# Kernel optimization log

Hardware: AMD Instinct MI355X
Metric: run time of the kernel (lower is better)

Reference implementation:

```python
import jax, jax.numpy as jnp
import numpy as np

B, S, H = 64, 256, 768          # batch, seq, feature_size
A = 8                            # atten_num (heads)
GNUM, GSZ = 8192, 64             # group_num, labels per group
LABELS = GNUM * GSZ              # 524288
E = 256                          # args.hidden_size (label embed dim)
TOPK = 10                        # candidates_topk


def setup_inputs() -> dict:
    key = jax.random.key(0)
    ks = jax.random.split(key, 6)
    sc = lambda d: 1.0 / np.sqrt(d)
    return {
        "inputs": jax.random.normal(ks[0], (B, S, H), jnp.float32),
        "W_att": jax.random.normal(ks[1], (A, H), jnp.float32) * sc(H),
        "b_att": jnp.zeros((A,), jnp.float32),
        "W_clf": jax.random.normal(ks[2], (GNUM, H), jnp.float32) * sc(H),
        "b_clf": jnp.zeros((GNUM,), jnp.float32),
        "W_enc": jax.random.normal(ks[3], (E, H), jnp.float32) * sc(H),
        "b_enc": jnp.zeros((E,), jnp.float32),
        "embed_table": jax.random.normal(ks[4], (LABELS, E), jnp.float32) * sc(E),
        "group_y": jnp.arange(LABELS, dtype=jnp.int32).reshape(GNUM, GSZ),
    }


def reference(inputs, W_att, b_att, W_clf, b_clf, W_enc, b_enc, embed_table, group_y):
    # MulitAttention: [B,S,H] -> atten [B,A,S] -> softmax over S -> out [B,A,H]
    atten = jnp.einsum("bsh,ah->bas", inputs, W_att) + b_att[None, :, None]
    atten_sm = jax.nn.softmax(atten, axis=-1)
    out = jnp.einsum("bas,bsh->bah", atten_sm, inputs)

    # group classifier + MaxPool1d over heads -> c_out [B, GNUM]
    group_logits = jnp.einsum("bah,gh->bag", out, W_clf) + b_clf
    c_out = jnp.max(group_logits, axis=1)

    # get_candidates (inference path): sigmoid on detached logits, topk groups,
    # gather group members (fixed group size -> regular [B, TOPK*GSZ])
    probs = jax.nn.sigmoid(jax.lax.stop_gradient(c_out))
    scores, indices = jax.lax.top_k(probs, TOPK)            # [B, TOPK]
    candidates = group_y[indices].reshape(B, TOPK * GSZ)    # [B, C]
    group_candidates_scores = jnp.repeat(scores, GSZ, axis=1)  # [B, C]

    # label scoring: encoder(out) [B,A,E], embed gather [B,C,E],
    # batched dot products [B,A,C], maxpool over heads -> l_out [B,C]
    emb = jnp.einsum("bah,eh->bae", out, W_enc) + b_enc
    embed_weights = embed_table[candidates]                 # [B, C, E]
    logits = jnp.einsum("bce,bae->bac", embed_weights, emb)
    l_out = jnp.max(logits, axis=1)

    return c_out, l_out, candidates, group_candidates_scores
```

## Files before the change

kernel.cpp:

```cpp
#include <hip/hip_runtime.h>

#define B_    64
#define S_    256
#define H_    768
#define A_    8
#define GNUM_ 8192
#define GSZ_  64
#define E_    256
#define TOPK_ 10
#define C_    (TOPK_*GSZ_)
#define BROWS (GNUM_ + E_)

typedef short  bf16x8 __attribute__((ext_vector_type(8)));
typedef float  f32x4  __attribute__((ext_vector_type(4)));

__device__ __forceinline__ ushort f2bf(float x) {
    union { float f; unsigned u; } c; c.f = x;
    unsigned r = c.u + 0x7fff + ((c.u >> 16) & 1);
    return (ushort)(r >> 16);
}
__device__ __forceinline__ float bf2f(ushort h) {
    union { float f; unsigned u; } c; c.u = ((unsigned)h) << 16;
    return c.f;
}
__device__ __forceinline__ float asf(unsigned u) {
    union { unsigned u; float f; } c; c.u = u; return c.f;
}
__device__ __forceinline__ unsigned cvt_pk_bf16(float a, float b) {
    unsigned r;
    asm("v_cvt_pk_bf16_f32 %0, %1, %2" : "=v"(r) : "v"(a), "v"(b));
    return r;
}

__global__ __launch_bounds__(256) void attn1_kernel(
    const float* __restrict__ x, const float* __restrict__ Watt,
    const float* __restrict__ batt, float* __restrict__ attT)
{
    const int b  = blockIdx.x;
    const int s0 = blockIdx.y * 64;
    const int t  = threadIdx.x;
    const int sl = t & 63;
    const int g  = __builtin_amdgcn_readfirstlane(t >> 6);
    __shared__ float Xt[64][65];
    __shared__ float Pp[8][64][5];

    const float* xb = x + ((size_t)b * S_ + s0) * H_;
    float acc[A_] = {};

    for (int h0 = 0; h0 < H_; h0 += 64) {
        __syncthreads();
#pragma unroll
        for (int i = 0; i < 4; i++) {
            int fid = i * 256 + t;
            int r = fid >> 4;
            int c = (fid & 15) * 4;
            float4 v = *(const float4*)(xb + (size_t)r * H_ + h0 + c);
            Xt[r][c] = v.x; Xt[r][c+1] = v.y; Xt[r][c+2] = v.z; Xt[r][c+3] = v.w;
        }
        __syncthreads();
        const float* wp = Watt + h0 + g * 16;
#pragma unroll
        for (int h = 0; h < 16; h++) {
            float xv = Xt[sl][g * 16 + h];
#pragma unroll
            for (int a = 0; a < A_; a++) acc[a] += xv * wp[a * H_ + h];
        }
    }
#pragma unroll
    for (int a = 0; a < A_; a++) Pp[a][sl][g] = acc[a];
    __syncthreads();
#pragma unroll
    for (int i = 0; i < 2; i++) {
        int idx = i * 256 + t;
        int a = idx >> 6, s = idx & 63;
        float v = Pp[a][s][0] + Pp[a][s][1] + Pp[a][s][2] + Pp[a][s][3] + batt[a];
        attT[(size_t)b * (S_*A_) + (size_t)(s0 + s) * A_ + a] = v;
    }
}

__global__ __launch_bounds__(256) void attn2s_kernel(
    const float* __restrict__ x, const float* __restrict__ attT,
    ushort* __restrict__ Ah, ushort* __restrict__ Al)
{
    const int b = blockIdx.x, h0 = blockIdx.y * 256, t = threadIdx.x;
    __shared__ float La[S_ * A_];
    __shared__ float Wsm[A_][260];

#pragma unroll
    for (int i = 0; i < 2; i++) {
        int fid = i * 256 + t;
        *(float4*)&La[fid * 4] =
            *(const float4*)(attT + (size_t)b * (S_*A_) + (size_t)fid * 4);
    }
    __syncthreads();

    {
        const int a = t >> 5, l = t & 31;
        float mx = -1e30f;
#pragma unroll
        for (int k = 0; k < 8; k++) mx = fmaxf(mx, La[(l + 32*k) * A_ + a]);
#pragma unroll
        for (int off = 16; off >= 1; off >>= 1) mx = fmaxf(mx, __shfl_xor(mx, off));
        float ev[8]; float sm = 0.f;
#pragma unroll
        for (int k = 0; k < 8; k++) { ev[k] = expf(La[(l + 32*k) * A_ + a] - mx); sm += ev[k]; }
#pragma unroll
        for (int off = 16; off >= 1; off >>= 1) sm += __shfl_xor(sm, off);
        float inv = 1.f / sm;
#pragma unroll
        for (int k = 0; k < 8; k++) Wsm[a][l + 32*k] = ev[k] * inv;
    }
    __syncthreads();

    const float* xb = x + (size_t)b * S_ * H_ + h0 + t;
    float o[A_] = {};
    for (int s0 = 0; s0 < S_; s0 += 4) {
        float xv0 = xb[(size_t)(s0 + 0) * H_];
        float xv1 = xb[(size_t)(s0 + 1) * H_];
        float xv2 = xb[(size_t)(s0 + 2) * H_];
        float xv3 = xb[(size_t)(s0 + 3) * H_];
#pragma unroll
        for (int a = 0; a < A_; a++) {
            float4 w = *(const float4*)&Wsm[a][s0];
            o[a] += w.x * xv0 + w.y * xv1 + w.z * xv2 + w.w * xv3;
        }
    }
#pragma unroll
    for (int a = 0; a < A_; a++) {
        float v = o[a];
        ushort hi = f2bf(v);
        ushort lo = f2bf(v - bf2f(hi));
        size_t off = (size_t)(b * 8 + a) * H_ + h0 + t;
        Ah[off] = hi; Al[off] = lo;
    }
}

__global__ __launch_bounds__(256, 1) void gemm_mfma_kernel(
    const ushort* __restrict__ Ah, const ushort* __restrict__ Al,
    const float* __restrict__ Wclf, const float* __restrict__ Wenc,
    const float* __restrict__ bclf, const float* __restrict__ benc,
    float* __restrict__ c_out, float* __restrict__ emb)
{
    const int f = blockIdx.x;
    const int xcd = f & 7, s = f >> 3;
    const int p = xcd + 8 * (s >> 2);
    const int m = s & 3;
    if (p >= BROWS / 128) return;
    const int n0 = p * 128, m0 = m * 128;

    __shared__ __align__(16) ushort lds[2][4][128 * 32];
    const int t = threadIdx.x;
    const int w = t >> 6, l = t & 63;
    const int mq = (w & 1) * 64, nq = (w >> 1) * 64;

    const int srow = t >> 2, skc = t & 3;
    const int wr_idx = ((srow * 32 + skc * 8) ^ ((srow & 7) << 3));
    const ushort* baseAh = Ah + (size_t)m0 * H_;
    const ushort* baseAl = Al + (size_t)m0 * H_;
    const float*  baseB  = (n0 < GNUM_) ? (Wclf + (size_t)n0 * H_)
                                        : (Wenc + (size_t)(n0 - GNUM_) * H_);

    uint4  stA[2][2];
    float4 stB[2][2];
    auto loadk = [&](int k0) {
        size_t oA = (size_t)srow * H_ + k0 + skc * 8;
        stA[0][0] = *(const uint4*)(baseAh + oA);
        stA[0][1] = *(const uint4*)(baseAh + oA + (size_t)64 * H_);
        stA[1][0] = *(const uint4*)(baseAl + oA);
        stA[1][1] = *(const uint4*)(baseAl + oA + (size_t)64 * H_);
        const float* bp0 = baseB + (size_t)srow * H_ + k0 + skc * 8;
        const float* bp1 = bp0 + (size_t)64 * H_;
        stB[0][0] = *(const float4*)(bp0);
        stB[0][1] = *(const float4*)(bp0 + 4);
        stB[1][0] = *(const float4*)(bp1);
        stB[1][1] = *(const float4*)(bp1 + 4);
    };

    f32x4 acc[4][4] = {};
    loadk(0);
    const int kc = l >> 4, lr = l & 15;

    for (int kt = 0; kt < H_ / 32; ++kt) {
        ushort* bufp = &lds[kt & 1][0][0];
#pragma unroll
        for (int xx = 0; xx < 2; xx++) {
            *(uint4*)(bufp + xx * 4096 + wr_idx)        = stA[xx][0];
            *(uint4*)(bufp + xx * 4096 + 2048 + wr_idx) = stA[xx][1];
        }
#pragma unroll
        for (int rp = 0; rp < 2; rp++) {
            float fv[8] = { stB[rp][0].x, stB[rp][0].y, stB[rp][0].z, stB[rp][0].w,
                            stB[rp][1].x, stB[rp][1].y, stB[rp][1].z, stB[rp][1].w };
            uint4 hi, lo;
            unsigned* hip = (unsigned*)&hi;
            unsigned* lop = (unsigned*)&lo;
#pragma unroll
            for (int j = 0; j < 4; j++) {
                unsigned pk = cvt_pk_bf16(fv[2*j], fv[2*j+1]);
                hip[j] = pk;
                float r0 = fv[2*j]   - asf(pk << 16);
                float r1 = fv[2*j+1] - asf(pk & 0xffff0000u);
                lop[j] = cvt_pk_bf16(r0, r1);
            }
            *(uint4*)(bufp + 2 * 4096 + rp * 2048 + wr_idx) = hi;
            *(uint4*)(bufp + 3 * 4096 + rp * 2048 + wr_idx) = lo;
        }
        __syncthreads();
        if (kt + 1 < H_ / 32) loadk((kt + 1) * 32);

        bf16x8 fah[4], fal[4], fbh[4], fbl[4];
#pragma unroll
        for (int mt = 0; mt < 4; mt++) {
            int r = mq + mt * 16 + lr;
            int idx = ((r * 32 + kc * 8) ^ ((r & 7) << 3));
            fah[mt] = *(const bf16x8*)(bufp + idx);
            fal[mt] = *(const bf16x8*)(bufp + 4096 + idx);
        }
#pragma unroll
        for (int nt = 0; nt < 4; nt++) {
            int r = nq + nt * 16 + lr;
            int idx = ((r * 32 + kc * 8) ^ ((r & 7) << 3));
            fbh[nt] = *(const bf16x8*)(bufp + 2 * 4096 + idx);
            fbl[nt] = *(const bf16x8*)(bufp + 3 * 4096 + idx);
        }
#pragma unroll
        for (int mt = 0; mt < 4; mt++)
#pragma unroll
            for (int nt = 0; nt < 4; nt++) {
                acc[mt][nt] = __builtin_amdgcn_mfma_f32_16x16x32_bf16(fah[mt], fbh[nt], acc[mt][nt], 0, 0, 0);
                acc[mt][nt] = __builtin_amdgcn_mfma_f32_16x16x32_bf16(fal[mt], fbh[nt], acc[mt][nt], 0, 0, 0);
                acc[mt][nt] = __builtin_amdgcn_mfma_f32_16x16x32_bf16(fah[mt], fbl[nt], acc[mt][nt], 0, 0, 0);
            }
    }

    const int q = l >> 4;
    if (n0 < GNUM_) {
#pragma unroll
        for (int mt = 0; mt < 4; mt++)
#pragma unroll
            for (int nt = 0; nt < 4; nt++) {
                f32x4 a = acc[mt][nt];
                float v = fmaxf(fmaxf(a[0], a[1]), fmaxf(a[2], a[3]));
                v = fmaxf(v, __shfl_xor(v, 16));
                if ((q & 1) == 0) {
                    int mg = m0 + mq + mt * 16 + (q >> 1) * 8;
                    int n  = n0 + nq + nt * 16 + lr;
                    c_out[(size_t)(mg >> 3) * GNUM_ + n] = v + bclf[n];
                }
            }
    } else {
#pragma unroll
        for (int mt = 0; mt < 4; mt++)
#pragma unroll
            for (int nt = 0; nt < 4; nt++) {
                int n = n0 - GNUM_ + nq + nt * 16 + lr;
                float bn = benc[n];
#pragma unroll
                for (int r2 = 0; r2 < 4; r2++) {
                    int mg = m0 + mq + mt * 16 + q * 4 + r2;
                    emb[(size_t)mg * E_ + n] = acc[mt][nt][r2] + bn;
                }
            }
    }
}

__global__ __launch_bounds__(256) void topk_kernel(
    const float* __restrict__ c_out, const int* __restrict__ gy,
    float* __restrict__ cand_f, float* __restrict__ gcs, int* __restrict__ cand_i)
{
    const int b = blockIdx.x, t = threadIdx.x;
    const int lane = t & 63, wv = t >> 6;
    __shared__ float bvv[4]; __shared__ int bii[4];
    __shared__ float topv[TOPK_]; __shared__ int topi[TOPK_];

    const float* row = c_out + (size_t)b * GNUM_;
    float lv[TOPK_]; int li[TOPK_];
#pragma unroll
    for (int k = 0; k < TOPK_; k++) { lv[k] = -1.f; li[k] = 0x7fffffff; }

    for (int i = t; i < GNUM_; i += 256) {
        float p = 1.f / (1.f + expf(-row[i]));
        if (p > lv[TOPK_ - 1]) {
            float cv = p; int ci = i;
#pragma unroll
            for (int k = 0; k < TOPK_; k++) {
                bool sw = (cv > lv[k]);
                float tv = sw ? lv[k] : cv; int ti = sw ? li[k] : ci;
                lv[k] = sw ? cv : lv[k];    li[k] = sw ? ci : li[k];
                cv = tv; ci = ti;
            }
        }
    }

    for (int rnd = 0; rnd < TOPK_; rnd++) {
        float bv = lv[0]; int bi = li[0];
#pragma unroll
        for (int off = 32; off >= 1; off >>= 1) {
            float ov = __shfl_xor(bv, off); int oi = __shfl_xor(bi, off);
            if (ov > bv || (ov == bv && oi < bi)) { bv = ov; bi = oi; }
        }
        if (lane == 0) { bvv[wv] = bv; bii[wv] = bi; }
        __syncthreads();
        float gbv = bvv[0]; int gbi = bii[0];
#pragma unroll
        for (int w = 1; w < 4; w++) {
            float ov = bvv[w]; int oi = bii[w];
            if (ov > gbv || (ov == gbv && oi < gbi)) { gbv = ov; gbi = oi; }
        }
        if (t == 0) { topv[rnd] = gbv; topi[rnd] = gbi; }
        if (li[0] == gbi) {
#pragma unroll
            for (int k = 0; k < TOPK_ - 1; k++) { lv[k] = lv[k + 1]; li[k] = li[k + 1]; }
            lv[TOPK_ - 1] = -1.f; li[TOPK_ - 1] = 0x7fffffff;
        }
        __syncthreads();
    }

    for (int j = t; j < C_; j += 256) {
        int k = j >> 6, slot = j & 63;
        int gi = topi[k];
        int lbl = gy[gi * GSZ_ + slot];
        cand_f[(size_t)b * C_ + j] = (float)lbl;
        gcs[(size_t)b * C_ + j] = topv[k];
        cand_i[b * C_ + j] = lbl;
    }
}

__global__ __launch_bounds__(256) void score_kernel(
    const float* __restrict__ embw, const float* __restrict__ et,
    const int* __restrict__ cand, float* __restrict__ l_out)
{
    const int b = blockIdx.x, c00 = blockIdx.y * 64, t = threadIdx.x;
    __shared__ float el[A_ * E_];
#pragma unroll
    for (int i = 0; i < 2; i++) {
        int fid = i * 256 + t;
        *(float4*)&el[fid * 4] = *(const float4*)(embw + (size_t)b * (A_*E_) + fid * 4);
    }
    __syncthreads();
    const int lane = t & 63, wv = t >> 6, q = lane >> 4, sub = lane & 15;

    int c = c00 + wv * 4 + q;
    const float* er = et + (size_t)cand[b * C_ + c] * E_ + sub * 4;
    float4 v0 = *(const float4*)(er);
    float4 v1 = *(const float4*)(er + 64);
    float4 v2 = *(const float4*)(er + 128);
    float4 v3 = *(const float4*)(er + 192);

    for (int it = 0; it < 4; it++) {
        float4 n0, n1, n2, n3;
        if (it + 1 < 4) {
            int cn = c00 + (it + 1) * 16 + wv * 4 + q;
            const float* ern = et + (size_t)cand[b * C_ + cn] * E_ + sub * 4;
            n0 = *(const float4*)(ern);
            n1 = *(const float4*)(ern + 64);
            n2 = *(const float4*)(ern + 128);
            n3 = *(const float4*)(ern + 192);
        }
        float best = -1e30f;
#pragma unroll
        for (int a = 0; a < A_; a++) {
            const float* ep = el + a * E_ + sub * 4;
            float4 w0 = *(const float4*)(ep);
            float4 w1 = *(const float4*)(ep + 64);
            float4 w2 = *(const float4*)(ep + 128);
            float4 w3 = *(const float4*)(ep + 192);
            float p = v0.x*w0.x + v0.y*w0.y + v0.z*w0.z + v0.w*w0.w
                    + v1.x*w1.x + v1.y*w1.y + v1.z*w1.z + v1.w*w1.w
                    + v2.x*w2.x + v2.y*w2.y + v2.z*w2.z + v2.w*w2.w
                    + v3.x*w3.x + v3.y*w3.y + v3.z*w3.z + v3.w*w3.w;
#pragma unroll
            for (int off = 8; off >= 1; off >>= 1) p += __shfl_xor(p, off);
            best = fmaxf(best, p);
        }
        if (sub == 0) l_out[(size_t)b * C_ + c00 + it * 16 + wv * 4 + q] = best;
        v0 = n0; v1 = n1; v2 = n2; v3 = n3;
    }
}

extern "C" void kernel_launch(void* const* d_in, const int* in_sizes, int n_in,
                              void* d_out, int out_size, void* d_ws, size_t ws_size,
                              hipStream_t stream)
{
    (void)in_sizes; (void)n_in; (void)out_size; (void)ws_size;
    const float* x    = (const float*)d_in[0];
    const float* Watt = (const float*)d_in[1];
    const float* batt = (const float*)d_in[2];
    const float* Wclf = (const float*)d_in[3];
    const float* bclf = (const float*)d_in[4];
    const float* Wenc = (const float*)d_in[5];
    const float* benc = (const float*)d_in[6];
    const float* et   = (const float*)d_in[7];
    const int*   gy   = (const int*)d_in[8];

    float* out    = (float*)d_out;
    float* c_out  = out;
    float* l_out  = out + (size_t)B_ * GNUM_;
    float* cand_f = l_out + (size_t)B_ * C_;
    float* gcs    = cand_f + (size_t)B_ * C_;

    char* ws = (char*)d_ws;
    float*  attT  = (float*) (ws);
    float*  embw  = (float*) (ws + 524288);
    int*    candi = (int*)   (ws + 1048576);
    ushort* Ahw   = (ushort*)(ws + 1212416);
    ushort* Alw   = (ushort*)(ws + 1998848);

    attn1_kernel<<<dim3(B_, 4), 256, 0, stream>>>(x, Watt, batt, attT);
    attn2s_kernel<<<dim3(B_, 3), 256, 0, stream>>>(x, attT, Ahw, Alw);
    gemm_mfma_kernel<<<288, 256, 0, stream>>>(Ahw, Alw, Wclf, Wenc, bclf, benc, c_out, embw);
    topk_kernel<<<B_, 256, 0, stream>>>(c_out, gy, cand_f, gcs, candi);
    score_kernel<<<dim3(B_, 10), 256, 0, stream>>>(embw, et, candi, l_out);
}
```

Measured before the change: 153.9 us.

## Fuse per-tile top-k into GEMM epilogue, merge topk with scoring, add prefetching

The GEMM epilogue now computes sigmoid and a per-128-column top-10 for each batch row and writes the partial candidates. A new scoretop kernel merges the 64 partial lists per batch, gathers the candidates and scores them, replacing the separate topk and score kernels. The GEMM grid shrinks to 256 blocks, and the 8 encoder tiles are claimed through an atomic work queue whose counter is reset in attn1. attn1 and attn2s gain register prefetching of x. This removes a full pass over c_out and one launch, but adds serial warp-level top-k work to the GEMM tail and repeats the top-k merge in each of the 4 blocks per batch.

```diff
diff --git a/kernel.cpp b/kernel.cpp
--- a/kernel.cpp
+++ b/kernel.cpp
@@ -9,7 +9,6 @@
 #define E_    256
 #define TOPK_ 10
 #define C_    (TOPK_*GSZ_)
-#define BROWS (GNUM_ + E_)
 
 typedef short  bf16x8 __attribute__((ext_vector_type(8)));
 typedef float  f32x4  __attribute__((ext_vector_type(4)));
@@ -34,11 +33,14 @@
 
 __global__ __launch_bounds__(256) void attn1_kernel(
     const float* __restrict__ x, const float* __restrict__ Watt,
-    const float* __restrict__ batt, float* __restrict__ attT)
+    const float* __restrict__ batt, float* __restrict__ attT,
+    unsigned* __restrict__ qcnt)
 {
     const int b  = blockIdx.x;
     const int s0 = blockIdx.y * 64;
     const int t  = threadIdx.x;
+    if (b == 0 && blockIdx.y == 0 && t == 0)
+        __hip_atomic_store(qcnt, 0u, __ATOMIC_RELAXED, __HIP_MEMORY_SCOPE_AGENT);
     const int sl = t & 63;
     const int g  = __builtin_amdgcn_readfirstlane(t >> 6);
     __shared__ float Xt[64][65];
@@ -46,18 +48,30 @@
 
     const float* xb = x + ((size_t)b * S_ + s0) * H_;
     float acc[A_] = {};
-
+    int pr[4], pc[4];
+    float4 pref[4];
+#pragma unroll
+    for (int i = 0; i < 4; i++) {
+        int fid = i * 256 + t;
+        pr[i] = fid >> 4; pc[i] = (fid & 15) * 4;
+    }
+#pragma unroll
+    for (int i = 0; i < 4; i++)
+        pref[i] = *(const float4*)(xb + (size_t)pr[i] * H_ + pc[i]);
     for (int h0 = 0; h0 < H_; h0 += 64) {
         __syncthreads();
 #pragma unroll
         for (int i = 0; i < 4; i++) {
-            int fid = i * 256 + t;
-            int r = fid >> 4;
-            int c = (fid & 15) * 4;
-            float4 v = *(const float4*)(xb + (size_t)r * H_ + h0 + c);
-            Xt[r][c] = v.x; Xt[r][c+1] = v.y; Xt[r][c+2] = v.z; Xt[r][c+3] = v.w;
+            float4 v = pref[i];
+            float* dst = &Xt[pr[i]][pc[i]];
+            dst[0] = v.x; dst[1] = v.y; dst[2] = v.z; dst[3] = v.w;
         }
         __syncthreads();
+        if (h0 + 64 < H_) {
+#pragma unroll
+            for (int i = 0; i < 4; i++)
+                pref[i] = *(const float4*)(xb + (size_t)pr[i] * H_ + h0 + 64 + pc[i]);
+        }
         const float* wp = Watt + h0 + g * 16;
 #pragma unroll
         for (int h = 0; h < 16; h++) {
@@ -72,9 +86,9 @@
 #pragma unroll
     for (int i = 0; i < 2; i++) {
         int idx = i * 256 + t;
-        int a = idx >> 6, s = idx & 63;
-        float v = Pp[a][s][0] + Pp[a][s][1] + Pp[a][s][2] + Pp[a][s][3] + batt[a];
-        attT[(size_t)b * (S_*A_) + (size_t)(s0 + s) * A_ + a] = v;
+        int a = idx >> 6, s2 = idx & 63;
+        float v = Pp[a][s2][0] + Pp[a][s2][1] + Pp[a][s2][2] + Pp[a][s2][3] + batt[a];
+        attT[(size_t)b * (S_*A_) + (size_t)(s0 + s2) * A_ + a] = v;
     }
 }
 
@@ -84,7 +98,7 @@
 {
     const int b = blockIdx.x, h0 = blockIdx.y * 256, t = threadIdx.x;
     __shared__ float La[S_ * A_];
-    __shared__ float Wsm[A_][260];
+    __shared__ float Wm[A_][260];
 
 #pragma unroll
     for (int i = 0; i < 2; i++) {
@@ -93,7 +107,6 @@
             *(const float4*)(attT + (size_t)b * (S_*A_) + (size_t)fid * 4);
     }
     __syncthreads();
-
     {
         const int a = t >> 5, l = t & 31;
         float mx = -1e30f;
@@ -108,23 +121,31 @@
         for (int off = 16; off >= 1; off >>= 1) sm += __shfl_xor(sm, off);
         float inv = 1.f / sm;
 #pragma unroll
-        for (int k = 0; k < 8; k++) Wsm[a][l + 32*k] = ev[k] * inv;
+        for (int k = 0; k < 8; k++) Wm[a][l + 32*k] = ev[k] * inv;
     }
     __syncthreads();
 
     const float* xb = x + (size_t)b * S_ * H_ + h0 + t;
     float o[A_] = {};
-    for (int s0 = 0; s0 < S_; s0 += 4) {
-        float xv0 = xb[(size_t)(s0 + 0) * H_];
-        float xv1 = xb[(size_t)(s0 + 1) * H_];
-        float xv2 = xb[(size_t)(s0 + 2) * H_];
-        float xv3 = xb[(size_t)(s0 + 3) * H_];
-#pragma unroll
-        for (int a = 0; a < A_; a++) {
-            float4 w = *(const float4*)&Wsm[a][s0];
-            o[a] += w.x * xv0 + w.y * xv1 + w.z * xv2 + w.w * xv3;
-        }
-    }
+    float xb0[16], xb1[16];
+#define LOADSTRIP(buf, ks) { _Pragma("unroll") \
+    for (int i = 0; i < 16; i++) buf[i] = xb[(size_t)((ks)*16 + i) * H_]; }
+#define COMPSTRIP(buf, ks) { _Pragma("unroll") \
+    for (int sg = 0; sg < 4; sg++) { _Pragma("unroll") \
+        for (int a = 0; a < A_; a++) { \
+            float4 w2 = *(const float4*)&Wm[a][(ks)*16 + sg*4]; \
+            o[a] += w2.x*buf[sg*4+0] + w2.y*buf[sg*4+1] \
+                  + w2.z*buf[sg*4+2] + w2.w*buf[sg*4+3]; } } }
+    LOADSTRIP(xb0, 0)
+#pragma unroll
+    for (int kp = 0; kp < 8; kp++) {
+        LOADSTRIP(xb1, 2*kp + 1)
+        COMPSTRIP(xb0, 2*kp)
+        if (kp < 7) LOADSTRIP(xb0, 2*kp + 2)
+        COMPSTRIP(xb1, 2*kp + 1)
+    }
+#undef LOADSTRIP
+#undef COMPSTRIP
 #pragma unroll
     for (int a = 0; a < A_; a++) {
         float v = o[a];
@@ -139,149 +160,199 @@
     const ushort* __restrict__ Ah, const ushort* __restrict__ Al,
     const float* __restrict__ Wclf, const float* __restrict__ Wenc,
     const float* __restrict__ bclf, const float* __restrict__ benc,
-    float* __restrict__ c_out, float* __restrict__ emb)
+    float* __restrict__ c_out, float* __restrict__ emb,
+    float* __restrict__ t10v, int* __restrict__ t10i,
+    unsigned* __restrict__ qcnt)
 {
-    const int f = blockIdx.x;
-    const int xcd = f & 7, s = f >> 3;
-    const int p = xcd + 8 * (s >> 2);
-    const int m = s & 3;
-    if (p >= BROWS / 128) return;
-    const int n0 = p * 128, m0 = m * 128;
-
     __shared__ __align__(16) ushort lds[2][4][128 * 32];
+    __shared__ unsigned jtile;
     const int t = threadIdx.x;
     const int w = t >> 6, l = t & 63;
     const int mq = (w & 1) * 64, nq = (w >> 1) * 64;
-
     const int srow = t >> 2, skc = t & 3;
     const int wr_idx = ((srow * 32 + skc * 8) ^ ((srow & 7) << 3));
-    const ushort* baseAh = Ah + (size_t)m0 * H_;
-    const ushort* baseAl = Al + (size_t)m0 * H_;
-    const float*  baseB  = (n0 < GNUM_) ? (Wclf + (size_t)n0 * H_)
-                                        : (Wenc + (size_t)(n0 - GNUM_) * H_);
-
-    uint4  stA[2][2];
-    float4 stB[2][2];
-    auto loadk = [&](int k0) {
-        size_t oA = (size_t)srow * H_ + k0 + skc * 8;
-        stA[0][0] = *(const uint4*)(baseAh + oA);
-        stA[0][1] = *(const uint4*)(baseAh + oA + (size_t)64 * H_);
-        stA[1][0] = *(const uint4*)(baseAl + oA);
-        stA[1][1] = *(const uint4*)(baseAl + oA + (size_t)64 * H_);
-        const float* bp0 = baseB + (size_t)srow * H_ + k0 + skc * 8;
-        const float* bp1 = bp0 + (size_t)64 * H_;
-        stB[0][0] = *(const float4*)(bp0);
-        stB[0][1] = *(const float4*)(bp0 + 4);
-        stB[1][0] = *(const float4*)(bp1);
-        stB[1][1] = *(const float4*)(bp1 + 4);
-    };
-
-    f32x4 acc[4][4] = {};
-    loadk(0);
     const int kc = l >> 4, lr = l & 15;
 
-    for (int kt = 0; kt < H_ / 32; ++kt) {
-        ushort* bufp = &lds[kt & 1][0][0];
-#pragma unroll
-        for (int xx = 0; xx < 2; xx++) {
-            *(uint4*)(bufp + xx * 4096 + wr_idx)        = stA[xx][0];
-            *(uint4*)(bufp + xx * 4096 + 2048 + wr_idx) = stA[xx][1];
-        }
-#pragma unroll
-        for (int rp = 0; rp < 2; rp++) {
-            float fv[8] = { stB[rp][0].x, stB[rp][0].y, stB[rp][0].z, stB[rp][0].w,
-                            stB[rp][1].x, stB[rp][1].y, stB[rp][1].z, stB[rp][1].w };
-            uint4 hi, lo;
-            unsigned* hip = (unsigned*)&hi;
-            unsigned* lop = (unsigned*)&lo;
-#pragma unroll
-            for (int j = 0; j < 4; j++) {
-                unsigned pk = cvt_pk_bf16(fv[2*j], fv[2*j+1]);
-                hip[j] = pk;
-                float r0 = fv[2*j]   - asf(pk << 16);
-                float r1 = fv[2*j+1] - asf(pk & 0xffff0000u);
-                lop[j] = cvt_pk_bf16(r0, r1);
-            }
-            *(uint4*)(bufp + 2 * 4096 + rp * 2048 + wr_idx) = hi;
-            *(uint4*)(bufp + 3 * 4096 + rp * 2048 + wr_idx) = lo;
-        }
-        __syncthreads();
-        if (kt + 1 < H_ / 32) loadk((kt + 1) * 32);
-
-        bf16x8 fah[4], fal[4], fbh[4], fbl[4];
-#pragma unroll
-        for (int mt = 0; mt < 4; mt++) {
-            int r = mq + mt * 16 + lr;
-            int idx = ((r * 32 + kc * 8) ^ ((r & 7) << 3));
-            fah[mt] = *(const bf16x8*)(bufp + idx);
-            fal[mt] = *(const bf16x8*)(bufp + 4096 + idx);
-        }
-#pragma unroll
-        for (int nt = 0; nt < 4; nt++) {
-            int r = nq + nt * 16 + lr;
-            int idx = ((r * 32 + kc * 8) ^ ((r & 7) << 3));
-            fbh[nt] = *(const bf16x8*)(bufp + 2 * 4096 + idx);
-            fbl[nt] = *(const bf16x8*)(bufp + 3 * 4096 + idx);
-        }
-#pragma unroll
-        for (int mt = 0; mt < 4; mt++)
+    int p = (blockIdx.x & 7) + 8 * ((blockIdx.x >> 3) >> 2);
+    int m = (blockIdx.x >> 3) & 3;
+
+    for (int iter = 0; ; iter++) {
+        if (iter > 0) {
+            __syncthreads();
+            if (t == 0) jtile = atomicAdd(qcnt, 1u);
+            __syncthreads();
+            unsigned j = jtile;
+            if (j >= 8u) break;
+            p = 64 + (int)(j >> 2);
+            m = (int)(j & 3);
+        }
+        const int n0 = p * 128, m0 = m * 128;
+        const ushort* baseAh = Ah + (size_t)m0 * H_;
+        const ushort* baseAl = Al + (size_t)m0 * H_;
+        const float*  baseB  = (n0 < GNUM_) ? (Wclf + (size_t)n0 * H_)
+                                            : (Wenc + (size_t)(n0 - GNUM_) * H_);
+        uint4  stA[2][2];
+        float4 stB[2][2];
+        auto loadk = [&](int k0) {
+            size_t oA = (size_t)srow * H_ + k0 + skc * 8;
+            stA[0][0] = *(const uint4*)(baseAh + oA);
+            stA[0][1] = *(const uint4*)(baseAh + oA + (size_t)64 * H_);
+            stA[1][0] = *(const uint4*)(baseAl + oA);
+            stA[1][1] = *(const uint4*)(baseAl + oA + (size_t)64 * H_);
+            const float* bp0 = baseB + (size_t)srow * H_ + k0 + skc * 8;
+            const float* bp1 = bp0 + (size_t)64 * H_;
+            stB[0][0] = *(const float4*)(bp0);
+            stB[0][1] = *(const float4*)(bp0 + 4);
+            stB[1][0] = *(const float4*)(bp1);
+            stB[1][1] = *(const float4*)(bp1 + 4);
+        };
+
+        f32x4 acc[4][4] = {};
+        loadk(0);
+
+        for (int kt = 0; kt < H_ / 32; ++kt) {
+            ushort* bufp = &lds[kt & 1][0][0];
+            if (iter > 0 && kt == 0) __syncthreads();
+#pragma unroll
+            for (int xx = 0; xx < 2; xx++) {
+                *(uint4*)(bufp + xx * 4096 + wr_idx)        = stA[xx][0];
+                *(uint4*)(bufp + xx * 4096 + 2048 + wr_idx) = stA[xx][1];
+            }
+#pragma unroll
+            for (int rp = 0; rp < 2; rp++) {
+                float fv[8] = { stB[rp][0].x, stB[rp][0].y, stB[rp][0].z, stB[rp][0].w,
+                                stB[rp][1].x, stB[rp][1].y, stB[rp][1].z, stB[rp][1].w };
+                uint4 hi, lo;
+                unsigned* hip = (unsigned*)&hi;
+                unsigned* lop = (unsigned*)&lo;
+#pragma unroll
+                for (int j2 = 0; j2 < 4; j2++) {
+                    unsigned pk = cvt_pk_bf16(fv[2*j2], fv[2*j2+1]);
+                    hip[j2] = pk;
+                    float r0 = fv[2*j2]   - asf(pk << 16);
+                    float r1 = fv[2*j2+1] - asf(pk & 0xffff0000u);
+                    lop[j2] = cvt_pk_bf16(r0, r1);
+                }
+                *(uint4*)(bufp + 2 * 4096 + rp * 2048 + wr_idx) = hi;
+                *(uint4*)(bufp + 3 * 4096 + rp * 2048 + wr_idx) = lo;
+            }
+            __syncthreads();
+            if (kt + 1 < H_ / 32) loadk((kt + 1) * 32);
+
+            bf16x8 fah[4], fal[4], fbh[4], fbl[4];
+#pragma unroll
+            for (int mt = 0; mt < 4; mt++) {
+                int r = mq + mt * 16 + lr;
+                int idx = ((r * 32 + kc * 8) ^ ((r & 7) << 3));
+                fah[mt] = *(const bf16x8*)(bufp + idx);
+                fal[mt] = *(const bf16x8*)(bufp + 4096 + idx);
+            }
 #pragma unroll
             for (int nt = 0; nt < 4; nt++) {
-                acc[mt][nt] = __builtin_amdgcn_mfma_f32_16x16x32_bf16(fah[mt], fbh[nt], acc[mt][nt], 0, 0, 0);
-                acc[mt][nt] = __builtin_amdgcn_mfma_f32_16x16x32_bf16(fal[mt], fbh[nt], acc[mt][nt], 0, 0, 0);
-                acc[mt][nt] = __builtin_amdgcn_mfma_f32_16x16x32_bf16(fah[mt], fbl[nt], acc[mt][nt], 0, 0, 0);
-            }
-    }
-
-    const int q = l >> 4;
-    if (n0 < GNUM_) {
-#pragma unroll
-        for (int mt = 0; mt < 4; mt++)
-#pragma unroll
-            for (int nt = 0; nt < 4; nt++) {
-                f32x4 a = acc[mt][nt];
-                float v = fmaxf(fmaxf(a[0], a[1]), fmaxf(a[2], a[3]));
-                v = fmaxf(v, __shfl_xor(v, 16));
-                if ((q & 1) == 0) {
-                    int mg = m0 + mq + mt * 16 + (q >> 1) * 8;
-                    int n  = n0 + nq + nt * 16 + lr;
-                    c_out[(size_t)(mg >> 3) * GNUM_ + n] = v + bclf[n];
+                int r = nq + nt * 16 + lr;
+                int idx = ((r * 32 + kc * 8) ^ ((r & 7) << 3));
+                fbh[nt] = *(const bf16x8*)(bufp + 2 * 4096 + idx);
+                fbl[nt] = *(const bf16x8*)(bufp + 3 * 4096 + idx);
+            }
+#pragma unroll
+            for (int mt = 0; mt < 4; mt++)
+#pragma unroll
+                for (int nt = 0; nt < 4; nt++) {
+                    acc[mt][nt] = __builtin_amdgcn_mfma_f32_16x16x32_bf16(fah[mt], fbh[nt], acc[mt][nt], 0, 0, 0);
+                    acc[mt][nt] = __builtin_amdgcn_mfma_f32_16x16x32_bf16(fal[mt], fbh[nt], acc[mt][nt], 0, 0, 0);
+                    acc[mt][nt] = __builtin_amdgcn_mfma_f32_16x16x32_bf16(fah[mt], fbl[nt], acc[mt][nt], 0, 0, 0);
                 }
-            }
-    } else {
-#pragma unroll
-        for (int mt = 0; mt < 4; mt++)
-#pragma unroll
-            for (int nt = 0; nt < 4; nt++) {
-                int n = n0 - GNUM_ + nq + nt * 16 + lr;
-                float bn = benc[n];
-#pragma unroll
-                for (int r2 = 0; r2 < 4; r2++) {
-                    int mg = m0 + mq + mt * 16 + q * 4 + r2;
-                    emb[(size_t)mg * E_ + n] = acc[mt][nt][r2] + bn;
+        }
+
+        const int q = l >> 4;
+        if (n0 < GNUM_) {
+            float* Pm = (float*)&lds[0][0][0];
+#pragma unroll
+            for (int mt = 0; mt < 4; mt++)
+#pragma unroll
+                for (int nt = 0; nt < 4; nt++) {
+                    f32x4 a = acc[mt][nt];
+                    float v = fmaxf(fmaxf(a[0], a[1]), fmaxf(a[2], a[3]));
+                    v = fmaxf(v, __shfl_xor(v, 16));
+                    if ((q & 1) == 0) {
+                        int r16 = (mq >> 3) + 2 * mt + (q >> 1);
+                        int col = nq + nt * 16 + lr;
+                        int n   = n0 + col;
+                        float logit = v + bclf[n];
+                        c_out[(size_t)((m0 >> 3) + r16) * GNUM_ + n] = logit;
+                        Pm[r16 * 128 + col] = 1.f / (1.f + expf(-logit));
+                    }
                 }
-            }
-    }
-}
-
-__global__ __launch_bounds__(256) void topk_kernel(
-    const float* __restrict__ c_out, const int* __restrict__ gy,
-    float* __restrict__ cand_f, float* __restrict__ gcs, int* __restrict__ cand_i)
+            __syncthreads();
+#pragma unroll
+            for (int rr = 0; rr < 4; rr++) {
+                int r = w * 4 + rr;
+                float p0 = Pm[r * 128 + l];
+                float p1 = Pm[r * 128 + 64 + l];
+                int bg = (m0 >> 3) + r;
+                size_t tb = ((size_t)bg * 64 + p) * TOPK_;
+                for (int k = 0; k < TOPK_; k++) {
+                    float bv; int bi;
+                    if (p0 >= p1) { bv = p0; bi = l; } else { bv = p1; bi = 64 + l; }
+#pragma unroll
+                    for (int off = 32; off >= 1; off >>= 1) {
+                        float ov = __shfl_xor(bv, off); int oi = __shfl_xor(bi, off);
+                        if (ov > bv || (ov == bv && oi < bi)) { bv = ov; bi = oi; }
+                    }
+                    if (l == 0) { t10v[tb + k] = bv; t10i[tb + k] = n0 + bi; }
+                    if (bi < 64) { if (l == bi) p0 = -1.f; }
+                    else         { if (l == bi - 64) p1 = -1.f; }
+                }
+            }
+        } else {
+#pragma unroll
+            for (int mt = 0; mt < 4; mt++)
+#pragma unroll
+                for (int nt = 0; nt < 4; nt++) {
+                    int n = n0 - GNUM_ + nq + nt * 16 + lr;
+                    float bn = benc[n];
+#pragma unroll
+                    for (int r2 = 0; r2 < 4; r2++) {
+                        int mg = m0 + mq + mt * 16 + q * 4 + r2;
+                        emb[(size_t)mg * E_ + n] = acc[mt][nt][r2] + bn;
+                    }
+                }
+        }
+    }
+}
+
+__global__ __launch_bounds__(256) void scoretop_kernel(
+    const float* __restrict__ t10v, const int* __restrict__ t10i,
+    const float* __restrict__ embw, const float* __restrict__ et,
+    const int* __restrict__ gy,
+    float* __restrict__ l_out, float* __restrict__ cand_f,
+    float* __restrict__ gcs)
 {
-    const int b = blockIdx.x, t = threadIdx.x;
-    const int lane = t & 63, wv = t >> 6;
+    const int b = blockIdx.x >> 2, q4 = blockIdx.x & 3, t = threadIdx.x;
+    __shared__ float el[A_ * E_];
+    __shared__ float tvs[640];
+    __shared__ int   tis[640];
     __shared__ float bvv[4]; __shared__ int bii[4];
     __shared__ float topv[TOPK_]; __shared__ int topi[TOPK_];
 
-    const float* row = c_out + (size_t)b * GNUM_;
+#pragma unroll
+    for (int i = 0; i < 2; i++) {
+        int fid = i * 256 + t;
+        *(float4*)&el[fid * 4] = *(const float4*)(embw + (size_t)b * (A_*E_) + fid * 4);
+    }
+    for (int j = t; j < 640; j += 256) {
+        tvs[j] = t10v[(size_t)b * 640 + j];
+        tis[j] = t10i[(size_t)b * 640 + j];
+    }
+    __syncthreads();
+
     float lv[TOPK_]; int li[TOPK_];
 #pragma unroll
     for (int k = 0; k < TOPK_; k++) { lv[k] = -1.f; li[k] = 0x7fffffff; }
-
-    for (int i = t; i < GNUM_; i += 256) {
-        float p = 1.f / (1.f + expf(-row[i]));
-        if (p > lv[TOPK_ - 1]) {
-            float cv = p; int ci = i;
+    for (int j = t; j < 640; j += 256) {
+        float pv = tvs[j]; int gi = tis[j];
+        if (pv > lv[TOPK_ - 1]) {
+            float cv = pv; int ci = gi;
 #pragma unroll
             for (int k = 0; k < TOPK_; k++) {
                 bool sw = (cv > lv[k]);
@@ -291,7 +362,7 @@
             }
         }
     }
-
+    const int lane = t & 63, wv = t >> 6;
     for (int rnd = 0; rnd < TOPK_; rnd++) {
         float bv = lv[0]; int bi = li[0];
 #pragma unroll
@@ -303,8 +374,8 @@
         __syncthreads();
         float gbv = bvv[0]; int gbi = bii[0];
 #pragma unroll
-        for (int w = 1; w < 4; w++) {
-            float ov = bvv[w]; int oi = bii[w];
+        for (int w2 = 1; w2 < 4; w2++) {
+            float ov = bvv[w2]; int oi = bii[w2];
             if (ov > gbv || (ov == gbv && oi < gbi)) { gbv = ov; gbi = oi; }
         }
         if (t == 0) { topv[rnd] = gbv; topi[rnd] = gbi; }
@@ -316,46 +387,33 @@
         __syncthreads();
     }
 
-    for (int j = t; j < C_; j += 256) {
-        int k = j >> 6, slot = j & 63;
-        int gi = topi[k];
-        int lbl = gy[gi * GSZ_ + slot];
-        cand_f[(size_t)b * C_ + j] = (float)lbl;
-        gcs[(size_t)b * C_ + j] = topv[k];
-        cand_i[b * C_ + j] = lbl;
-    }
-}
-
-__global__ __launch_bounds__(256) void score_kernel(
-    const float* __restrict__ embw, const float* __restrict__ et,
-    const int* __restrict__ cand, float* __restrict__ l_out)
-{
-    const int b = blockIdx.x, c00 = blockIdx.y * 64, t = threadIdx.x;
-    __shared__ float el[A_ * E_];
-#pragma unroll
-    for (int i = 0; i < 2; i++) {
-        int fid = i * 256 + t;
-        *(float4*)&el[fid * 4] = *(const float4*)(embw + (size_t)b * (A_*E_) + fid * 4);
-    }
-    __syncthreads();
-    const int lane = t & 63, wv = t >> 6, q = lane >> 4, sub = lane & 15;
-
-    int c = c00 + wv * 4 + q;
-    const float* er = et + (size_t)cand[b * C_ + c] * E_ + sub * 4;
+    const int cbase = q4 * 160;
+    if (t < 160) {
+        int c = cbase + t;
+        int k = c >> 6, slot = c & 63;
+        int lbl = gy[topi[k] * GSZ_ + slot];
+        cand_f[(size_t)b * C_ + c] = (float)lbl;
+        gcs[(size_t)b * C_ + c] = topv[k];
+    }
+
+    const int qq = lane >> 4, sub = lane & 15;
+    int c = cbase + wv * 4 + qq;
+    int lbl0 = gy[topi[c >> 6] * GSZ_ + (c & 63)];
+    const float* er = et + (size_t)lbl0 * E_ + sub * 4;
     float4 v0 = *(const float4*)(er);
     float4 v1 = *(const float4*)(er + 64);
     float4 v2 = *(const float4*)(er + 128);
     float4 v3 = *(const float4*)(er + 192);
-
-    for (int it = 0; it < 4; it++) {
-        float4 n0, n1, n2, n3;
-        if (it + 1 < 4) {
-            int cn = c00 + (it + 1) * 16 + wv * 4 + q;
-            const float* ern = et + (size_t)cand[b * C_ + cn] * E_ + sub * 4;
-            n0 = *(const float4*)(ern);
-            n1 = *(const float4*)(ern + 64);
-            n2 = *(const float4*)(ern + 128);
-            n3 = *(const float4*)(ern + 192);
+    for (int pass = 0; pass < 10; pass++) {
+        float4 p0, p1, p2, p3;
+        if (pass + 1 < 10) {
+            int cn = cbase + (pass + 1) * 16 + wv * 4 + qq;
+            int lbln = gy[topi[cn >> 6] * GSZ_ + (cn & 63)];
+            const float* ern = et + (size_t)lbln * E_ + sub * 4;
+            p0 = *(const float4*)(ern);
+            p1 = *(const float4*)(ern + 64);
+            p2 = *(const float4*)(ern + 128);
+            p3 = *(const float4*)(ern + 192);
         }
         float best = -1e30f;
 #pragma unroll
@@ -365,16 +423,16 @@
             float4 w1 = *(const float4*)(ep + 64);
             float4 w2 = *(const float4*)(ep + 128);
             float4 w3 = *(const float4*)(ep + 192);
-            float p = v0.x*w0.x + v0.y*w0.y + v0.z*w0.z + v0.w*w0.w
-                    + v1.x*w1.x + v1.y*w1.y + v1.z*w1.z + v1.w*w1.w
-                    + v2.x*w2.x + v2.y*w2.y + v2.z*w2.z + v2.w*w2.w
-                    + v3.x*w3.x + v3.y*w3.y + v3.z*w3.z + v3.w*w3.w;
-#pragma unroll
-            for (int off = 8; off >= 1; off >>= 1) p += __shfl_xor(p, off);
-            best = fmaxf(best, p);
-        }
-        if (sub == 0) l_out[(size_t)b * C_ + c00 + it * 16 + wv * 4 + q] = best;
-        v0 = n0; v1 = n1; v2 = n2; v3 = n3;
+            float pp = v0.x*w0.x + v0.y*w0.y + v0.z*w0.z + v0.w*w0.w
+                     + v1.x*w1.x + v1.y*w1.y + v1.z*w1.z + v1.w*w1.w
+                     + v2.x*w2.x + v2.y*w2.y + v2.z*w2.z + v2.w*w2.w
+                     + v3.x*w3.x + v3.y*w3.y + v3.z*w3.z + v3.w*w3.w;
+#pragma unroll
+            for (int off = 8; off >= 1; off >>= 1) pp += __shfl_xor(pp, off);
+            best = fmaxf(best, pp);
+        }
+        if (sub == 0) l_out[(size_t)b * C_ + cbase + pass * 16 + wv * 4 + qq] = best;
+        v0 = p0; v1 = p1; v2 = p2; v3 = p3;
     }
 }
 
@@ -400,15 +458,18 @@
     float* gcs    = cand_f + (size_t)B_ * C_;
 
     char* ws = (char*)d_ws;
-    float*  attT  = (float*) (ws);
-    float*  embw  = (float*) (ws + 524288);
-    int*    candi = (int*)   (ws + 1048576);
-    ushort* Ahw   = (ushort*)(ws + 1212416);
-    ushort* Alw   = (ushort*)(ws + 1998848);
-
-    attn1_kernel<<<dim3(B_, 4), 256, 0, stream>>>(x, Watt, batt, attT);
+    float*    attT = (float*)   (ws);
+    float*    embw = (float*)   (ws + 524288);
+    ushort*   Ahw  = (ushort*)  (ws + 1048576);
+    ushort*   Alw  = (ushort*)  (ws + 1835008);
+    float*    t10v = (float*)   (ws + 2621440);
+    int*      t10i = (int*)     (ws + 2785280);
+    unsigned* qcnt = (unsigned*)(ws + 2949120);
+
+    attn1_kernel<<<dim3(B_, 4), 256, 0, stream>>>(x, Watt, batt, attT, qcnt);
     attn2s_kernel<<<dim3(B_, 3), 256, 0, stream>>>(x, attT, Ahw, Alw);
-    gemm_mfma_kernel<<<288, 256, 0, stream>>>(Ahw, Alw, Wclf, Wenc, bclf, benc, c_out, embw);
-    topk_kernel<<<B_, 256, 0, stream>>>(c_out, gy, cand_f, gcs, candi);
-    score_kernel<<<dim3(B_, 10), 256, 0, stream>>>(embw, et, candi, l_out);
-}
+    gemm_mfma_kernel<<<256, 256, 0, stream>>>(Ahw, Alw, Wclf, Wenc, bclf, benc,
+                                              c_out, embw, t10v, t10i, qcnt);
+    scoretop_kernel<<<256, 256, 0, stream>>>(t10v, t10i, embw, et, gy,
+                                             l_out, cand_f, gcs);
+}
```

Result: slower. 229.5 us (+49.2%).
